# Optimization experiments

Measured on AMD Instinct MI355X. Metric: run time of the kernel, lower is better.

Reference implementation:

```python
import jax, jax.numpy as jnp
import numpy as np

B = 65536
IN = 64
H = 128
OUT = 2


def setup_inputs() -> dict:
    key = jax.random.key(0)
    ks = jax.random.split(key, 16)
    s_in = 1.0 / np.sqrt(IN)
    s_h = 1.0 / np.sqrt(H)
    d = {}
    d["x"] = jax.random.normal(ks[0], (B, IN), dtype=jnp.float32)
    # initial state (module resets to zeros per day)
    d["h0"] = jnp.zeros((H,), dtype=jnp.float32)
    d["c0"] = jnp.zeros((B, H), dtype=jnp.float32)
    # input->hidden linears (with bias), torch Linear layout [out, in]
    for i, name in enumerate(["f", "i", "o", "c"]):
        d[f"Wx{name}"] = jax.random.uniform(ks[1 + i], (H, IN), jnp.float32, -s_in, s_in)
        d[f"bx{name}"] = jax.random.uniform(ks[5 + i], (H,), jnp.float32, -s_in, s_in)
        d[f"Wh{name}"] = jax.random.uniform(ks[9 + i], (H, H), jnp.float32, -s_h, s_h)
    d["Wy"] = jax.random.uniform(ks[13], (OUT, H), jnp.float32, -s_h, s_h)
    d["by"] = jax.random.uniform(ks[14], (OUT,), jnp.float32, -s_h, s_h)
    return d


def reference(x, h0, c0, Wxf, bxf, Wxi, bxi, Wxo, bxo, Wxc, bxc, Whf, Whi, Who, Whc, Wy, by):
    # hidden recurrent contributions (h0 is a length-H vector, broadcast over batch)
    hi = h0 @ Whi.T  # [H]
    hf = h0 @ Whf.T
    ho = h0 @ Who.T
    hc = h0 @ Whc.T
    i = jax.nn.sigmoid(x @ Wxi.T + bxi + hi)  # [B, H]
    f = jax.nn.sigmoid(x @ Wxf.T + bxf + hf)
    o = jax.nn.sigmoid(x @ Wxo.T + bxo + ho)
    c_til = jnp.tanh(x @ Wxc.T + bxc + hc)
    c = f * c0 + i * c_til
    h = o * jnp.tanh(c)
    y_hat = h @ Wy.T + by  # [B, OUT]
    return y_hat
```

## Files before the change

### kernel.cpp

```cpp
#include <hip/hip_runtime.h>


#define B_SIZE 65536

typedef __bf16 bf16x8 __attribute__((ext_vector_type(8)));
typedef __bf16 bf16x4 __attribute__((ext_vector_type(4)));
typedef float f32x4 __attribute__((ext_vector_type(4)));

__device__ __forceinline__ float fsig(float x) {
    float e = __builtin_amdgcn_exp2f(-1.442695040888963f * x);
    return __builtin_amdgcn_rcpf(1.0f + e);
}
__device__ __forceinline__ float ftanh(float x) {
    float e = __builtin_amdgcn_exp2f(2.885390081777927f * x);
    return 1.0f - 2.0f * __builtin_amdgcn_rcpf(e + 1.0f);
}

__global__ void bias_kernel(const float* __restrict__ h0,
                            const float* __restrict__ Whf, const float* __restrict__ Whi,
                            const float* __restrict__ Who, const float* __restrict__ Whc,
                            const float* __restrict__ bxf, const float* __restrict__ bxi,
                            const float* __restrict__ bxo, const float* __restrict__ bxc,
                            float* __restrict__ bias512) {
    int j = blockIdx.x * 64 + threadIdx.x;
    int g = j >> 7, r = j & 127;
    const float* Wh = (g == 0) ? Whf : (g == 1) ? Whi : (g == 2) ? Who : Whc;
    const float* bx = (g == 0) ? bxf : (g == 1) ? bxi : (g == 2) ? bxo : bxc;
    float s = bx[r];
    const float4* row = (const float4*)(Wh + r * 128);
    const float4* h4  = (const float4*)h0;
#pragma unroll 8
    for (int k = 0; k < 32; ++k) {
        float4 a = row[k], b = h4[k];
        s += a.x * b.x + a.y * b.y + a.z * b.z + a.w * b.w;
    }
    bias512[j] = s;
}

__global__ void prep_kernel(const float* __restrict__ Wxf, const float* __restrict__ Wxi,
                            const float* __restrict__ Wxo, const float* __restrict__ Wxc,
                            __bf16* __restrict__ frags) {
    int t = blockIdx.x * 64 + threadIdx.x;
    int w    = t >> 10;
    int g    = (t >> 8) & 3;
    int cb   = (t >> 7) & 1;
    int kb   = (t >> 6) & 1;
    int lane = t & 63;
    const float* Wx = (g == 0) ? Wxf : (g == 1) ? Wxi : (g == 2) ? Wxo : Wxc;
    const int n = w * 32 + cb * 16 + (lane & 15);
    const float* p = Wx + n * 64 + kb * 32 + (lane >> 4) * 8;
    float4 lo = *(const float4*)p;
    float4 hi = *(const float4*)(p + 4);
    bf16x8 v;
    v[0] = (__bf16)lo.x; v[1] = (__bf16)lo.y; v[2] = (__bf16)lo.z; v[3] = (__bf16)lo.w;
    v[4] = (__bf16)hi.x; v[5] = (__bf16)hi.y; v[6] = (__bf16)hi.z; v[7] = (__bf16)hi.w;
    *(bf16x8*)(frags + (size_t)t * 8) = v;
}

__launch_bounds__(256, 2)
__global__ void lstm_kernel(const float* __restrict__ x, const float* __restrict__ c0,
                            const __bf16* __restrict__ frags,
                            const float* __restrict__ Wy, const float* __restrict__ by,
                            const float* __restrict__ bias512, float* __restrict__ out) {
    __shared__ __bf16 xs[2][1024];
    __shared__ float cs[2][16 * 132];
    __shared__ float yred[4][128][2];

    const int tid  = threadIdx.x;
    const int lane = tid & 63;
    const int w    = tid >> 6;
    const int q    = lane >> 4;
    const int n15  = lane & 15;

    bf16x8 bw[4][2][2];
    float biasv[4][2];
#pragma unroll
    for (int g = 0; g < 4; ++g)
#pragma unroll
        for (int cb = 0; cb < 2; ++cb) {
            biasv[g][cb] = bias512[g * 128 + w * 32 + cb * 16 + n15];
#pragma unroll
            for (int kb = 0; kb < 2; ++kb)
                bw[g][cb][kb] = *(const bf16x8*)(frags +
                    (size_t)(((w * 16 + g * 4 + cb * 2 + kb) * 64 + lane)) * 8);
        }
    float wyv[2][2];
#pragma unroll
    for (int o = 0; o < 2; ++o)
#pragma unroll
        for (int cb = 0; cb < 2; ++cb)
            wyv[o][cb] = Wy[o * 128 + w * 32 + cb * 16 + n15];
    const float by0 = by[0], by1 = by[1];

    constexpr int ITERS = (B_SIZE / 16) / 512;
    const int tile0 = blockIdx.x * ITERS;

    const int xrow = tid >> 4;
    const int k4   = (tid & 15) * 4;
    const int sidx = (k4 >> 5) * 512 + ((k4 & 31) >> 3) * 128 + xrow * 8 + (k4 & 7);

    const int ccol = (tid & 15) * 8;
    const int cidx = xrow * 132 + ccol;

    float4 xr  = *(const float4*)(x  + (size_t)(tile0 * 16 + xrow) * 64 + k4);
    float4 cpa = *(const float4*)(c0 + (size_t)(tile0 * 16 + xrow) * 128 + ccol);
    float4 cpb = *(const float4*)(c0 + (size_t)(tile0 * 16 + xrow) * 128 + ccol + 4);
    {
        bf16x4 v; v[0] = (__bf16)xr.x; v[1] = (__bf16)xr.y; v[2] = (__bf16)xr.z; v[3] = (__bf16)xr.w;
        *(bf16x4*)&xs[0][sidx] = v;
        *(float4*)&cs[0][cidx] = cpa;
        *(float4*)&cs[0][cidx + 4] = cpb;
    }
    xr  = *(const float4*)(x  + (size_t)((tile0 + 1) * 16 + xrow) * 64 + k4);
    cpa = *(const float4*)(c0 + (size_t)((tile0 + 1) * 16 + xrow) * 128 + ccol);
    cpb = *(const float4*)(c0 + (size_t)((tile0 + 1) * 16 + xrow) * 128 + ccol + 4);
    __syncthreads();

#pragma unroll
    for (int it = 0; it < ITERS; ++it) {
        const int cur = it & 1;

        bf16x8 a0 = *(const bf16x8*)&xs[cur][lane * 8];
        bf16x8 a1 = *(const bf16x8*)&xs[cur][512 + lane * 8];

        float c0v[2][4];
#pragma unroll
        for (int cb = 0; cb < 2; ++cb)
#pragma unroll
            for (int r = 0; r < 4; ++r)
                c0v[cb][r] = cs[cur][(q * 4 + r) * 132 + w * 32 + cb * 16 + n15];

        if (it + 1 < ITERS) {
            bf16x4 v; v[0] = (__bf16)xr.x; v[1] = (__bf16)xr.y; v[2] = (__bf16)xr.z; v[3] = (__bf16)xr.w;
            *(bf16x4*)&xs[cur ^ 1][sidx] = v;
            *(float4*)&cs[cur ^ 1][cidx] = cpa;
            *(float4*)&cs[cur ^ 1][cidx + 4] = cpb;
            if (it + 2 < ITERS) {
                const int tn = tile0 + it + 2;
                xr  = *(const float4*)(x  + (size_t)(tn * 16 + xrow) * 64 + k4);
                cpa = *(const float4*)(c0 + (size_t)(tn * 16 + xrow) * 128 + ccol);
                cpb = *(const float4*)(c0 + (size_t)(tn * 16 + xrow) * 128 + ccol + 4);
            }
        }

        f32x4 acc[4][2];
#pragma unroll
        for (int g = 0; g < 4; ++g)
#pragma unroll
            for (int cb = 0; cb < 2; ++cb) {
                float b = biasv[g][cb];
                f32x4 t = {b, b, b, b};
                acc[g][cb] = t;
            }
#pragma unroll
        for (int g = 0; g < 4; ++g)
#pragma unroll
            for (int cb = 0; cb < 2; ++cb) {
                acc[g][cb] = __builtin_amdgcn_mfma_f32_16x16x32_bf16(a0, bw[g][cb][0], acc[g][cb], 0, 0, 0);
                acc[g][cb] = __builtin_amdgcn_mfma_f32_16x16x32_bf16(a1, bw[g][cb][1], acc[g][cb], 0, 0, 0);
            }

        float p0[4] = {0.f, 0.f, 0.f, 0.f};
        float p1[4] = {0.f, 0.f, 0.f, 0.f};
#pragma unroll
        for (int cb = 0; cb < 2; ++cb)
#pragma unroll
            for (int r = 0; r < 4; ++r) {
                float fg = fsig(acc[0][cb][r]);
                float ig = fsig(acc[1][cb][r]);
                float og = fsig(acc[2][cb][r]);
                float ct = ftanh(acc[3][cb][r]);
                float c  = fg * c0v[cb][r] + ig * ct;
                float h  = og * ftanh(c);
                p0[r] += h * wyv[0][cb];
                p1[r] += h * wyv[1][cb];
            }
#pragma unroll
        for (int m = 1; m < 16; m <<= 1) {
#pragma unroll
            for (int r = 0; r < 4; ++r) {
                p0[r] += __shfl_xor(p0[r], m, 64);
                p1[r] += __shfl_xor(p1[r], m, 64);
            }
        }
        if (n15 == 0) {
#pragma unroll
            for (int r = 0; r < 4; ++r) {
                yred[w][it * 16 + q * 4 + r][0] = p0[r];
                yred[w][it * 16 + q * 4 + r][1] = p1[r];
            }
        }
        __syncthreads();
    }

    if (tid < 128) {
        float s0 = by0 + yred[0][tid][0] + yred[1][tid][0] + yred[2][tid][0] + yred[3][tid][0];
        float s1 = by1 + yred[0][tid][1] + yred[1][tid][1] + yred[2][tid][1] + yred[3][tid][1];
        float2 s = {s0, s1};
        *(float2*)(out + (size_t)(tile0 * 16 + tid) * 2) = s;
    }
}

extern "C" void kernel_launch(void* const* d_in, const int* in_sizes, int n_in,
                              void* d_out, int out_size, void* d_ws, size_t ws_size,
                              hipStream_t stream) {
    const float* x   = (const float*)d_in[0];
    const float* h0  = (const float*)d_in[1];
    const float* c0  = (const float*)d_in[2];
    const float* Wxf = (const float*)d_in[3];
    const float* bxf = (const float*)d_in[4];
    const float* Whf = (const float*)d_in[5];
    const float* Wxi = (const float*)d_in[6];
    const float* bxi = (const float*)d_in[7];
    const float* Whi = (const float*)d_in[8];
    const float* Wxo = (const float*)d_in[9];
    const float* bxo = (const float*)d_in[10];
    const float* Who = (const float*)d_in[11];
    const float* Wxc = (const float*)d_in[12];
    const float* bxc = (const float*)d_in[13];
    const float* Whc = (const float*)d_in[14];
    const float* Wy  = (const float*)d_in[15];
    const float* by  = (const float*)d_in[16];
    float* out = (float*)d_out;
    float* bias512 = (float*)d_ws;
    __bf16* frags  = (__bf16*)((float*)d_ws + 512);

    bias_kernel<<<8, 64, 0, stream>>>(h0, Whf, Whi, Who, Whc, bxf, bxi, bxo, bxc, bias512);
    prep_kernel<<<64, 64, 0, stream>>>(Wxf, Wxi, Wxo, Wxc, frags);
    lstm_kernel<<<512, 256, 0, stream>>>(x, c0, frags, Wy, by, bias512, out);
}
```

Baseline: 126.1 us.

## Merge prep kernels, fold exp scaling into weights, restructure prefetch and reduction

Fuses the bias and weight-fragment prep kernels into one launch to remove a kernel launch. The sigmoid and tanh exponent scale factors are folded into the bf16 weights and bias, which saves a multiply per gate element. Global prefetch is moved to the top of each iteration with double-buffered registers, and the shared-memory store of the next tile is moved after compute. The cross-lane shuffle reduction is shortened from 4 steps to 2, with partial sums written to a larger shared buffer and summed at the end. Scaling the weights before the bf16 cast changes rounding slightly.

New measurement: 128.5 us. Within noise of the previous version (+1.9%).

```diff
diff --git a/kernel.cpp b/kernel.cpp
--- a/kernel.cpp
+++ b/kernel.cpp
@@ -7,54 +7,57 @@
 typedef __bf16 bf16x4 __attribute__((ext_vector_type(4)));
 typedef float f32x4 __attribute__((ext_vector_type(4)));
 
-__device__ __forceinline__ float fsig(float x) {
-    float e = __builtin_amdgcn_exp2f(-1.442695040888963f * x);
-    return __builtin_amdgcn_rcpf(1.0f + e);
-}
+#define LOG2E 1.442695040888963f
+#define TWO_LOG2E 2.885390081777927f
+
 __device__ __forceinline__ float ftanh(float x) {
-    float e = __builtin_amdgcn_exp2f(2.885390081777927f * x);
+    float e = __builtin_amdgcn_exp2f(TWO_LOG2E * x);
     return 1.0f - 2.0f * __builtin_amdgcn_rcpf(e + 1.0f);
 }
 
-__global__ void bias_kernel(const float* __restrict__ h0,
+__global__ void prep_kernel(const float* __restrict__ h0,
                             const float* __restrict__ Whf, const float* __restrict__ Whi,
                             const float* __restrict__ Who, const float* __restrict__ Whc,
                             const float* __restrict__ bxf, const float* __restrict__ bxi,
                             const float* __restrict__ bxo, const float* __restrict__ bxc,
-                            float* __restrict__ bias512) {
-    int j = blockIdx.x * 64 + threadIdx.x;
-    int g = j >> 7, r = j & 127;
-    const float* Wh = (g == 0) ? Whf : (g == 1) ? Whi : (g == 2) ? Who : Whc;
-    const float* bx = (g == 0) ? bxf : (g == 1) ? bxi : (g == 2) ? bxo : bxc;
-    float s = bx[r];
-    const float4* row = (const float4*)(Wh + r * 128);
-    const float4* h4  = (const float4*)h0;
+                            const float* __restrict__ Wxf, const float* __restrict__ Wxi,
+                            const float* __restrict__ Wxo, const float* __restrict__ Wxc,
+                            float* __restrict__ bias512, __bf16* __restrict__ frags) {
+    if (blockIdx.x < 8) {
+        int j = blockIdx.x * 64 + threadIdx.x;
+        int g = j >> 7, r = j & 127;
+        const float* Wh = (g == 0) ? Whf : (g == 1) ? Whi : (g == 2) ? Who : Whc;
+        const float* bx = (g == 0) ? bxf : (g == 1) ? bxi : (g == 2) ? bxo : bxc;
+        const float sg = (g == 3) ? TWO_LOG2E : -LOG2E;
+        float s = bx[r];
+        const float4* row = (const float4*)(Wh + r * 128);
+        const float4* h4  = (const float4*)h0;
 #pragma unroll 8
-    for (int k = 0; k < 32; ++k) {
-        float4 a = row[k], b = h4[k];
-        s += a.x * b.x + a.y * b.y + a.z * b.z + a.w * b.w;
-    }
-    bias512[j] = s;
-}
-
-__global__ void prep_kernel(const float* __restrict__ Wxf, const float* __restrict__ Wxi,
-                            const float* __restrict__ Wxo, const float* __restrict__ Wxc,
-                            __bf16* __restrict__ frags) {
-    int t = blockIdx.x * 64 + threadIdx.x;
-    int w    = t >> 10;
-    int g    = (t >> 8) & 3;
-    int cb   = (t >> 7) & 1;
-    int kb   = (t >> 6) & 1;
-    int lane = t & 63;
-    const float* Wx = (g == 0) ? Wxf : (g == 1) ? Wxi : (g == 2) ? Wxo : Wxc;
-    const int n = w * 32 + cb * 16 + (lane & 15);
-    const float* p = Wx + n * 64 + kb * 32 + (lane >> 4) * 8;
-    float4 lo = *(const float4*)p;
-    float4 hi = *(const float4*)(p + 4);
-    bf16x8 v;
-    v[0] = (__bf16)lo.x; v[1] = (__bf16)lo.y; v[2] = (__bf16)lo.z; v[3] = (__bf16)lo.w;
-    v[4] = (__bf16)hi.x; v[5] = (__bf16)hi.y; v[6] = (__bf16)hi.z; v[7] = (__bf16)hi.w;
-    *(bf16x8*)(frags + (size_t)t * 8) = v;
+        for (int k = 0; k < 32; ++k) {
+            float4 a = row[k], b = h4[k];
+            s += a.x * b.x + a.y * b.y + a.z * b.z + a.w * b.w;
+        }
+        bias512[j] = s * sg;
+    } else {
+        int t = (blockIdx.x - 8) * 64 + threadIdx.x;
+        int w    = t >> 10;
+        int g    = (t >> 8) & 3;
+        int cb   = (t >> 7) & 1;
+        int kb   = (t >> 6) & 1;
+        int lane = t & 63;
+        const float* Wx = (g == 0) ? Wxf : (g == 1) ? Wxi : (g == 2) ? Wxo : Wxc;
+        const float sg = (g == 3) ? TWO_LOG2E : -LOG2E;
+        const int n = w * 32 + cb * 16 + (lane & 15);
+        const float* p = Wx + n * 64 + kb * 32 + (lane >> 4) * 8;
+        float4 lo = *(const float4*)p;
+        float4 hi = *(const float4*)(p + 4);
+        bf16x8 v;
+        v[0] = (__bf16)(lo.x * sg); v[1] = (__bf16)(lo.y * sg);
+        v[2] = (__bf16)(lo.z * sg); v[3] = (__bf16)(lo.w * sg);
+        v[4] = (__bf16)(hi.x * sg); v[5] = (__bf16)(hi.y * sg);
+        v[6] = (__bf16)(hi.z * sg); v[7] = (__bf16)(hi.w * sg);
+        *(bf16x8*)(frags + (size_t)t * 8) = v;
+    }
 }
 
 __launch_bounds__(256, 2)
@@ -64,7 +67,7 @@
                             const float* __restrict__ bias512, float* __restrict__ out) {
     __shared__ __bf16 xs[2][1024];
     __shared__ float cs[2][16 * 132];
-    __shared__ float yred[4][128][2];
+    __shared__ float yred[4][128][8];
 
     const int tid  = threadIdx.x;
     const int lane = tid & 63;
@@ -102,23 +105,35 @@
     const int ccol = (tid & 15) * 8;
     const int cidx = xrow * 132 + ccol;
 
-    float4 xr  = *(const float4*)(x  + (size_t)(tile0 * 16 + xrow) * 64 + k4);
-    float4 cpa = *(const float4*)(c0 + (size_t)(tile0 * 16 + xrow) * 128 + ccol);
-    float4 cpb = *(const float4*)(c0 + (size_t)(tile0 * 16 + xrow) * 128 + ccol + 4);
+    float4 xr[2], cpa[2], cpb[2];
+
+    xr[0]  = *(const float4*)(x  + (size_t)(tile0 * 16 + xrow) * 64 + k4);
+    cpa[0] = *(const float4*)(c0 + (size_t)(tile0 * 16 + xrow) * 128 + ccol);
+    cpb[0] = *(const float4*)(c0 + (size_t)(tile0 * 16 + xrow) * 128 + ccol + 4);
     {
-        bf16x4 v; v[0] = (__bf16)xr.x; v[1] = (__bf16)xr.y; v[2] = (__bf16)xr.z; v[3] = (__bf16)xr.w;
+        bf16x4 v; v[0] = (__bf16)xr[0].x; v[1] = (__bf16)xr[0].y;
+        v[2] = (__bf16)xr[0].z; v[3] = (__bf16)xr[0].w;
         *(bf16x4*)&xs[0][sidx] = v;
-        *(float4*)&cs[0][cidx] = cpa;
-        *(float4*)&cs[0][cidx + 4] = cpb;
-    }
-    xr  = *(const float4*)(x  + (size_t)((tile0 + 1) * 16 + xrow) * 64 + k4);
-    cpa = *(const float4*)(c0 + (size_t)((tile0 + 1) * 16 + xrow) * 128 + ccol);
-    cpb = *(const float4*)(c0 + (size_t)((tile0 + 1) * 16 + xrow) * 128 + ccol + 4);
+        *(float4*)&cs[0][cidx] = cpa[0];
+        *(float4*)&cs[0][cidx + 4] = cpb[0];
+    }
+    xr[0]  = *(const float4*)(x  + (size_t)((tile0 + 1) * 16 + xrow) * 64 + k4);
+    cpa[0] = *(const float4*)(c0 + (size_t)((tile0 + 1) * 16 + xrow) * 128 + ccol);
+    cpb[0] = *(const float4*)(c0 + (size_t)((tile0 + 1) * 16 + xrow) * 128 + ccol + 4);
     __syncthreads();
 
 #pragma unroll
     for (int it = 0; it < ITERS; ++it) {
         const int cur = it & 1;
+        const int hs  = it & 1;
+        const int fs  = hs ^ 1;
+
+        if (it + 2 < ITERS) {
+            const int tn = tile0 + it + 2;
+            xr[fs]  = *(const float4*)(x  + (size_t)(tn * 16 + xrow) * 64 + k4);
+            cpa[fs] = *(const float4*)(c0 + (size_t)(tn * 16 + xrow) * 128 + ccol);
+            cpb[fs] = *(const float4*)(c0 + (size_t)(tn * 16 + xrow) * 128 + ccol + 4);
+        }
 
         bf16x8 a0 = *(const bf16x8*)&xs[cur][lane * 8];
         bf16x8 a1 = *(const bf16x8*)&xs[cur][512 + lane * 8];
@@ -129,19 +144,6 @@
 #pragma unroll
             for (int r = 0; r < 4; ++r)
                 c0v[cb][r] = cs[cur][(q * 4 + r) * 132 + w * 32 + cb * 16 + n15];
-
-        if (it + 1 < ITERS) {
-            bf16x4 v; v[0] = (__bf16)xr.x; v[1] = (__bf16)xr.y; v[2] = (__bf16)xr.z; v[3] = (__bf16)xr.w;
-            *(bf16x4*)&xs[cur ^ 1][sidx] = v;
-            *(float4*)&cs[cur ^ 1][cidx] = cpa;
-            *(float4*)&cs[cur ^ 1][cidx + 4] = cpb;
-            if (it + 2 < ITERS) {
-                const int tn = tile0 + it + 2;
-                xr  = *(const float4*)(x  + (size_t)(tn * 16 + xrow) * 64 + k4);
-                cpa = *(const float4*)(c0 + (size_t)(tn * 16 + xrow) * 128 + ccol);
-                cpb = *(const float4*)(c0 + (size_t)(tn * 16 + xrow) * 128 + ccol + 4);
-            }
-        }
 
         f32x4 acc[4][2];
 #pragma unroll
@@ -166,36 +168,52 @@
         for (int cb = 0; cb < 2; ++cb)
 #pragma unroll
             for (int r = 0; r < 4; ++r) {
-                float fg = fsig(acc[0][cb][r]);
-                float ig = fsig(acc[1][cb][r]);
-                float og = fsig(acc[2][cb][r]);
-                float ct = ftanh(acc[3][cb][r]);
+                float fg = __builtin_amdgcn_rcpf(1.0f + __builtin_amdgcn_exp2f(acc[0][cb][r]));
+                float ig = __builtin_amdgcn_rcpf(1.0f + __builtin_amdgcn_exp2f(acc[1][cb][r]));
+                float og = __builtin_amdgcn_rcpf(1.0f + __builtin_amdgcn_exp2f(acc[2][cb][r]));
+                float ec = __builtin_amdgcn_exp2f(acc[3][cb][r]);
+                float ct = 1.0f - 2.0f * __builtin_amdgcn_rcpf(ec + 1.0f);
                 float c  = fg * c0v[cb][r] + ig * ct;
                 float h  = og * ftanh(c);
                 p0[r] += h * wyv[0][cb];
                 p1[r] += h * wyv[1][cb];
             }
 #pragma unroll
-        for (int m = 1; m < 16; m <<= 1) {
+        for (int m = 1; m < 4; m <<= 1) {
 #pragma unroll
             for (int r = 0; r < 4; ++r) {
                 p0[r] += __shfl_xor(p0[r], m, 64);
                 p1[r] += __shfl_xor(p1[r], m, 64);
             }
         }
-        if (n15 == 0) {
+        if ((n15 & 3) == 0) {
+            const int part = n15 >> 2;
 #pragma unroll
             for (int r = 0; r < 4; ++r) {
-                yred[w][it * 16 + q * 4 + r][0] = p0[r];
-                yred[w][it * 16 + q * 4 + r][1] = p1[r];
-            }
+                yred[w][it * 16 + q * 4 + r][part]     = p0[r];
+                yred[w][it * 16 + q * 4 + r][4 + part] = p1[r];
+            }
+        }
+
+        if (it + 1 < ITERS) {
+            bf16x4 v; v[0] = (__bf16)xr[hs].x; v[1] = (__bf16)xr[hs].y;
+            v[2] = (__bf16)xr[hs].z; v[3] = (__bf16)xr[hs].w;
+            *(bf16x4*)&xs[cur ^ 1][sidx] = v;
+            *(float4*)&cs[cur ^ 1][cidx] = cpa[hs];
+            *(float4*)&cs[cur ^ 1][cidx + 4] = cpb[hs];
         }
         __syncthreads();
     }
 
     if (tid < 128) {
-        float s0 = by0 + yred[0][tid][0] + yred[1][tid][0] + yred[2][tid][0] + yred[3][tid][0];
-        float s1 = by1 + yred[0][tid][1] + yred[1][tid][1] + yred[2][tid][1] + yred[3][tid][1];
+        float s0 = by0, s1 = by1;
+#pragma unroll
+        for (int w2 = 0; w2 < 4; ++w2)
+#pragma unroll
+            for (int p = 0; p < 4; ++p) {
+                s0 += yred[w2][tid][p];
+                s1 += yred[w2][tid][4 + p];
+            }
         float2 s = {s0, s1};
         *(float2*)(out + (size_t)(tile0 * 16 + tid) * 2) = s;
     }
@@ -225,7 +243,7 @@
     float* bias512 = (float*)d_ws;
     __bf16* frags  = (__bf16*)((float*)d_ws + 512);
 
-    bias_kernel<<<8, 64, 0, stream>>>(h0, Whf, Whi, Who, Whc, bxf, bxi, bxo, bxc, bias512);
-    prep_kernel<<<64, 64, 0, stream>>>(Wxf, Wxi, Wxo, Wxc, frags);
+    prep_kernel<<<72, 64, 0, stream>>>(h0, Whf, Whi, Who, Whc, bxf, bxi, bxo, bxc,
+                                       Wxf, Wxi, Wxo, Wxc, bias512, frags);
     lstm_kernel<<<512, 256, 0, stream>>>(x, c0, frags, Wy, by, bias512, out);
 }
```
